# Kernel tuning notes

Measured on AMD Instinct MI355X. Metric: run time of the kernel, lower is better.

## Reference

```python
import jax, jax.numpy as jnp
import numpy as np

S_DIM, T_DIM, FEAT_DIM = 2048, 2048, 128
NCE_N, NCE_T, NCE_MOM = 16384, 0.07, 0.5
N_DATA, BATCH = 100000, 64
EPS = 1e-7


def _l2norm(x):
    return x / jnp.linalg.norm(x, axis=1, keepdims=True)


def setup_inputs() -> dict:
    key = jax.random.key(0)
    ks = jax.random.split(key, 10)
    feat_s = jax.random.normal(ks[0], (BATCH, S_DIM), dtype=jnp.float32)
    feat_t = jax.random.normal(ks[1], (BATCH, T_DIM), dtype=jnp.float32)
    idx = jax.random.randint(ks[2], (BATCH,), 0, N_DATA)
    sample_idx = jax.random.randint(ks[3], (BATCH, NCE_N + 1), 0, N_DATA)
    sample_idx = sample_idx.at[:, 0].set(idx)  # positive sample in column 0
    # Embed linear weights (Linear(dim_in, feat_dim))
    w_s = jax.random.normal(ks[4], (FEAT_DIM, S_DIM), dtype=jnp.float32) / np.sqrt(S_DIM)
    b_s = jnp.zeros((FEAT_DIM,), dtype=jnp.float32)
    w_t = jax.random.normal(ks[5], (FEAT_DIM, T_DIM), dtype=jnp.float32) / np.sqrt(T_DIM)
    b_t = jnp.zeros((FEAT_DIM,), dtype=jnp.float32)
    # memory banks, uniform(-stdv, stdv), stdv = 1/sqrt(feat_dim/3)
    stdv = 1.0 / np.sqrt(FEAT_DIM / 3.0)
    mem_v1 = jax.random.uniform(ks[6], (N_DATA, FEAT_DIM), dtype=jnp.float32, minval=-stdv, maxval=stdv)
    mem_v2 = jax.random.uniform(ks[7], (N_DATA, FEAT_DIM), dtype=jnp.float32, minval=-stdv, maxval=stdv)
    return {"feat_s": feat_s, "feat_t": feat_t, "idx": idx, "sample_idx": sample_idx,
            "w_s": w_s, "b_s": b_s, "w_t": w_t, "b_t": b_t,
            "mem_v1": mem_v1, "mem_v2": mem_v2}


def _contrast_out(mem, samp_idx, v):
    # gather [B, K+1, D] from memory bank, bmm against [B, D]
    w = mem[samp_idx]                                # [B, K+1, D]
    logits = jnp.einsum('bkd,bd->bk', w, v) / NCE_T  # [B, K+1]
    out = jnp.exp(logits)
    z = jnp.mean(out) * N_DATA                       # first-pass Z estimate
    return out / z


def _contrast_loss(x):
    b = x.shape[0]
    m = float(NCE_N) / N_DATA
    log_d1 = jnp.log(x[:, 0] / (x[:, 0] + m + EPS))          # positives
    log_d0 = jnp.log(m / (x[:, 1:] + m + EPS))               # negatives
    return -(jnp.sum(log_d1) + jnp.sum(log_d0)) / b


def reference(feat_s, feat_t, idx, sample_idx, w_s, b_s, w_t, b_t, mem_v1, mem_v2):
    hs = _l2norm(feat_s @ w_s.T + b_s)  # [B, D]
    ht = _l2norm(feat_t @ w_t.T + b_t)  # [B, D]
    out_s = _contrast_out(mem_v2, sample_idx, hs)  # anchor=student vs teacher memory
    out_t = _contrast_out(mem_v1, sample_idx, ht)  # anchor=teacher vs student memory
    return _contrast_loss(out_s) + _contrast_loss(out_t)
```

## Files before the change

### kernel.cpp

```cpp
#include <hip/hip_runtime.h>

#define DIM_IN   2048
#define FEAT     128
#define KP1      16385
#define NDATA    100000
#define BATCH    64
#define NBG      64
#define NTG      ((NDATA + NBG - 1) / NBG)
#define GCH      32
#define LCH      8

constexpr float NCE_T_INV = 1.0f / 0.07f;
constexpr float M_CONST   = 16384.0f / 100000.0f;
constexpr float EPS_C     = 1e-7f;

typedef short bf16x8 __attribute__((ext_vector_type(8)));
typedef float f32x4  __attribute__((ext_vector_type(4)));

#define VP_PLANE 34816
#define VP_SIDE  17408
#define VP_ROW   272

__global__ void __launch_bounds__(1024) embed_kernel(
    const float* __restrict__ feat_s, const float* __restrict__ feat_t,
    const float* __restrict__ w_s, const float* __restrict__ b_s,
    const float* __restrict__ w_t, const float* __restrict__ b_t,
    char* __restrict__ vplanes, float* __restrict__ z_zero,
    float* __restrict__ out_zero)
{
    const int blk  = blockIdx.x;
    const int side = blk >> 6;
    const int b    = blk & 63;
    const float* feat = (side == 0 ? feat_s : feat_t) + (size_t)b * DIM_IN;
    const float* w    = (side == 0 ? w_s : w_t);
    const float* bias = (side == 0 ? b_s : b_t);

    __shared__ float sfeat[DIM_IN];
    __shared__ float pre[FEAT];
    __shared__ float wsum[2];

    const int t = threadIdx.x;
    if (blk == 0) {
        if (t < 128) z_zero[t] = 0.f;
        else if (t == 128) out_zero[0] = 0.f;
    }
    {
        const float4* f4 = (const float4*)feat;
        float4* s4 = (float4*)sfeat;
        if (t < 512) s4[t] = f4[t];
    }
    __syncthreads();

    const int wv = t >> 6, ln = t & 63;
    const float4* w4  = (const float4*)w;
    const float4* sf4 = (const float4*)sfeat;
#pragma unroll 2
    for (int i = 0; i < 8; ++i) {
        const int d = wv + i * 16;
        float s = 0.f;
#pragma unroll
        for (int seg = 0; seg < 8; ++seg) {
            float4 a = w4[d * (DIM_IN / 4) + seg * 64 + ln];
            float4 f = sf4[seg * 64 + ln];
            s += a.x * f.x + a.y * f.y + a.z * f.z + a.w * f.w;
        }
#pragma unroll
        for (int o = 32; o > 0; o >>= 1) s += __shfl_xor(s, o, 64);
        if (ln == 0) pre[d] = s;
    }
    __syncthreads();

    if (t < 128) {
        float p = pre[t] + bias[t];
        pre[t] = p;
        float sq = p * p;
#pragma unroll
        for (int o = 32; o > 0; o >>= 1) sq += __shfl_xor(sq, o, 64);
        if ((t & 63) == 0) wsum[t >> 6] = sq;
    }
    __syncthreads();
    if (t < 128) {
        float inv_norm = 1.0f / sqrtf(wsum[0] + wsum[1]);
        float x = pre[t] * inv_norm;
        unsigned int u = __float_as_uint(x);
        unsigned short h = (unsigned short)(u >> 16);
        float hf = __uint_as_float(u & 0xffff0000u);
        float lr = x - hf;
        unsigned short l = (unsigned short)(__float_as_uint(lr) >> 16);
        const size_t off = (size_t)side * VP_SIDE + (size_t)b * VP_ROW + t * 2;
        *(unsigned short*)(vplanes + off)            = h;
        *(unsigned short*)(vplanes + VP_PLANE + off) = l;
    }
}

__global__ void __launch_bounds__(512) gemm_exp_kernel(
    const float* __restrict__ mem_v1, const float* __restrict__ mem_v2,
    const char* __restrict__ vplanes, float* __restrict__ E)
{
    __shared__ __align__(16) char lds[67584];

    const int bx   = blockIdx.x;
    const int side = bx & 1;
    const int tile = bx >> 1;
    const int n0   = tile * NBG;
    const float* bank = (side == 0 ? mem_v2 : mem_v1);
    const int t  = threadIdx.x;
    const int wv = t >> 6, ln = t & 63;
    const int lm = ln & 15;
    const int kb = ln >> 4;
    const int ntile = wv & 3;
    const int mhalf = wv >> 2;
    const int nloc  = ntile * 16 + lm;

    {
        const size_t bmax = (size_t)NDATA * 512 - 16;
        const char* bbase = (const char*)bank;
        for (int s = wv; s < 32; s += 8) {
            const int o   = s * 1024 + ln * 16;
            const int row = o >> 9;
            const int so  = (o & ~511) | ((o & 511) ^ ((row & 7) << 4));
            size_t g = (size_t)n0 * 512 + so;
            if (g > bmax) g = bmax;
            __builtin_amdgcn_global_load_lds(
                (const __attribute__((address_space(1))) void*)(bbase + g),
                (__attribute__((address_space(3))) void*)(lds + 34816 + s * 1024),
                16, 0, 0);
        }
    }
    {
        const char* hbase = vplanes + (size_t)side * VP_SIDE;
        const char* lbase = vplanes + VP_PLANE + (size_t)side * VP_SIDE;
        for (int seg = wv; seg < 34; seg += 8) {
            const char* src = (seg < 17 ? hbase + seg * 1024
                                        : lbase + (seg - 17) * 1024) + ln * 16;
            __builtin_amdgcn_global_load_lds(
                (const __attribute__((address_space(1))) void*)src,
                (__attribute__((address_space(3))) void*)(lds + seg * 1024),
                16, 0, 0);
        }
    }

    f32x4 acc[2];
    acc[0] = (f32x4){0.f, 0.f, 0.f, 0.f};
    acc[1] = (f32x4){0.f, 0.f, 0.f, 0.f};

    __syncthreads();

    const int sw = (nloc & 7) << 4;
#pragma unroll
    for (int c = 0; c < 4; ++c) {
        const int bofs = nloc * 512 + c * 128 + kb * 32;
        const float4 f0 = *(const float4*)(lds + 34816 + ((bofs)      ^ sw));
        const float4 f1 = *(const float4*)(lds + 34816 + ((bofs + 16) ^ sw));
        const float xs[8] = {f0.x, f0.y, f0.z, f0.w, f1.x, f1.y, f1.z, f1.w};
        bf16x8 bh, bl;
#pragma unroll
        for (int j = 0; j < 8; ++j) {
            unsigned int u = __float_as_uint(xs[j]);
            bh[j] = (short)(u >> 16);
            float hf = __uint_as_float(u & 0xffff0000u);
            bl[j] = (short)(__float_as_uint(xs[j] - hf) >> 16);
        }
#pragma unroll
        for (int i = 0; i < 2; ++i) {
            const int mi = mhalf * 2 + i;
            bf16x8 ah = *(const bf16x8*)(lds + (mi * 16 + lm) * VP_ROW + c * 64 + kb * 16);
            bf16x8 al = *(const bf16x8*)(lds + 17408 + (mi * 16 + lm) * VP_ROW + c * 64 + kb * 16);
            acc[i] = __builtin_amdgcn_mfma_f32_16x16x32_bf16(ah, bh, acc[i], 0, 0, 0);
            acc[i] = __builtin_amdgcn_mfma_f32_16x16x32_bf16(al, bh, acc[i], 0, 0, 0);
            acc[i] = __builtin_amdgcn_mfma_f32_16x16x32_bf16(ah, bl, acc[i], 0, 0, 0);
        }
    }

    const int nn = n0 + nloc;
    if (nn < NDATA) {
#pragma unroll
        for (int i = 0; i < 2; ++i) {
            const int mi = mhalf * 2 + i;
#pragma unroll
            for (int jj = 0; jj < 4; ++jj) {
                const int anchor = mi * 16 + kb * 4 + jj;
                E[(size_t)(side * 64 + anchor) * NDATA + nn] =
                    __expf(acc[i][jj] * NCE_T_INV);
            }
        }
    }
}

__global__ void __launch_bounds__(256) gather_z_kernel(
    const int* __restrict__ sample_idx, const float* __restrict__ E,
    float* __restrict__ ex_out, float* __restrict__ z_out)
{
    const int blk   = blockIdx.x;
    const int chunk = blk >> 7;
    const int sb    = blk & 127;
    const int b     = sb & 63;
    const float* Eb = E + (size_t)sb * NDATA;

    float zp = 0.f;
    for (int k = chunk * 256 + threadIdx.x; k < KP1; k += GCH * 256) {
        const int idx = sample_idx[(size_t)b * KP1 + k];
        const float e = Eb[idx];
        ex_out[(size_t)sb * KP1 + k] = e;
        zp += e;
    }
#pragma unroll
    for (int o = 32; o > 0; o >>= 1) zp += __shfl_xor(zp, o, 64);
    __shared__ float zw[4];
    if ((threadIdx.x & 63) == 0) zw[threadIdx.x >> 6] = zp;
    __syncthreads();
    if (threadIdx.x == 0) atomicAdd(&z_out[sb], zw[0] + zw[1] + zw[2] + zw[3]);
}

__global__ void __launch_bounds__(256) loss_kernel(
    const float* __restrict__ ex_in, const float* __restrict__ z_in,
    float* __restrict__ out)
{
    const int blk   = blockIdx.x;
    const int chunk = blk >> 7;
    const int sb    = blk & 127;
    const int side  = sb >> 6;

    __shared__ float zsh;
    if (threadIdx.x < 64) {
        float zv = z_in[side * 64 + threadIdx.x];
#pragma unroll
        for (int o = 32; o > 0; o >>= 1) zv += __shfl_xor(zv, o, 64);
        if (threadIdx.x == 0) zsh = zv;
    }
    __syncthreads();

    const float z  = zsh * ((float)NDATA / (64.0f * (float)KP1));
    const float rz = 1.0f / z;
    const float* ex = ex_in + (size_t)sb * KP1;

    float part = 0.f;
    for (int k = chunk * 256 + threadIdx.x; k < KP1; k += LCH * 256) {
        const float x = ex[k] * rz;
        if (k == 0) part += __logf(x / (x + M_CONST + EPS_C));
        else        part += __logf(M_CONST / (x + M_CONST + EPS_C));
    }
#pragma unroll
    for (int o = 32; o > 0; o >>= 1) part += __shfl_xor(part, o, 64);
    __shared__ float pw[4];
    if ((threadIdx.x & 63) == 0) pw[threadIdx.x >> 6] = part;
    __syncthreads();
    if (threadIdx.x == 0)
        atomicAdd(out, -(pw[0] + pw[1] + pw[2] + pw[3]) * (1.0f / 64.0f));
}

extern "C" void kernel_launch(void* const* d_in, const int* in_sizes, int n_in,
                              void* d_out, int out_size, void* d_ws, size_t ws_size,
                              hipStream_t stream)
{
    const float* feat_s     = (const float*)d_in[0];
    const float* feat_t     = (const float*)d_in[1];
    const int*   sample_idx = (const int*)  d_in[3];
    const float* w_s        = (const float*)d_in[4];
    const float* b_s        = (const float*)d_in[5];
    const float* w_t        = (const float*)d_in[6];
    const float* b_t        = (const float*)d_in[7];
    const float* mem_v1     = (const float*)d_in[8];
    const float* mem_v2     = (const float*)d_in[9];
    float* out = (float*)d_out;

    char*  ws     = (char*)d_ws;
    float* ws_z   = (float*)ws;
    float* ws_ex  = (float*)(ws + 512);
    char*  ws_vp  = (char*)(ws + 512);
    float* ws_E   = (float*)(ws + 512 + (size_t)2 * BATCH * KP1 * sizeof(float));

    embed_kernel<<<2 * BATCH, 1024, 0, stream>>>(feat_s, feat_t, w_s, b_s, w_t, b_t,
                                                 ws_vp, ws_z, out);
    gemm_exp_kernel<<<2 * NTG, 512, 0, stream>>>(mem_v1, mem_v2, ws_vp, ws_E);
    gather_z_kernel<<<2 * BATCH * GCH, 256, 0, stream>>>(sample_idx, ws_E, ws_ex, ws_z);
    loss_kernel<<<2 * BATCH * LCH, 256, 0, stream>>>(ws_ex, ws_z, out);
}
```

Measured before the change: 205.7 us.

## Shrink GEMM tile to 32 rows and share sample indices across both sides

The GEMM-exp kernel now processes 32 memory-bank rows per block with 256 threads instead of 64 rows with 512 threads, and drops the bounds clamp because 32 divides NDATA evenly. This gives more, smaller blocks with less LDS each, but every block still reloads the full 34 KB vplane tile, so the vplane traffic per row doubles. The gather and loss kernels now handle both sides (student and teacher) in one block per batch row, so each sample index is loaded once and used for two E lookups. This halves index reads and block count, at the cost of more work per thread.

```diff
diff --git a/kernel.cpp b/kernel.cpp
--- a/kernel.cpp
+++ b/kernel.cpp
@@ -5,8 +5,8 @@
 #define KP1      16385
 #define NDATA    100000
 #define BATCH    64
-#define NBG      64
-#define NTG      ((NDATA + NBG - 1) / NBG)
+#define NBG      32
+#define NTG      (NDATA / NBG)
 #define GCH      32
 #define LCH      8
 
@@ -93,11 +93,11 @@
     }
 }
 
-__global__ void __launch_bounds__(512) gemm_exp_kernel(
+__global__ void __launch_bounds__(256) gemm_exp_kernel(
     const float* __restrict__ mem_v1, const float* __restrict__ mem_v2,
     const char* __restrict__ vplanes, float* __restrict__ E)
 {
-    __shared__ __align__(16) char lds[67584];
+    __shared__ __align__(16) char lds[51200];
 
     const int bx   = blockIdx.x;
     const int side = bx & 1;
@@ -108,19 +108,17 @@
     const int wv = t >> 6, ln = t & 63;
     const int lm = ln & 15;
     const int kb = ln >> 4;
-    const int ntile = wv & 3;
-    const int mhalf = wv >> 2;
+    const int ntile = wv & 1;
+    const int mpair = wv >> 1;
     const int nloc  = ntile * 16 + lm;
 
     {
-        const size_t bmax = (size_t)NDATA * 512 - 16;
         const char* bbase = (const char*)bank;
-        for (int s = wv; s < 32; s += 8) {
+        for (int s = wv; s < 16; s += 4) {
             const int o   = s * 1024 + ln * 16;
             const int row = o >> 9;
             const int so  = (o & ~511) | ((o & 511) ^ ((row & 7) << 4));
-            size_t g = (size_t)n0 * 512 + so;
-            if (g > bmax) g = bmax;
+            const size_t g = (size_t)n0 * 512 + so;
             __builtin_amdgcn_global_load_lds(
                 (const __attribute__((address_space(1))) void*)(bbase + g),
                 (__attribute__((address_space(3))) void*)(lds + 34816 + s * 1024),
@@ -130,7 +128,7 @@
     {
         const char* hbase = vplanes + (size_t)side * VP_SIDE;
         const char* lbase = vplanes + VP_PLANE + (size_t)side * VP_SIDE;
-        for (int seg = wv; seg < 34; seg += 8) {
+        for (int seg = wv; seg < 34; seg += 4) {
             const char* src = (seg < 17 ? hbase + seg * 1024
                                         : lbase + (seg - 17) * 1024) + ln * 16;
             __builtin_amdgcn_global_load_lds(
@@ -163,7 +161,7 @@
         }
 #pragma unroll
         for (int i = 0; i < 2; ++i) {
-            const int mi = mhalf * 2 + i;
+            const int mi = mpair * 2 + i;
             bf16x8 ah = *(const bf16x8*)(lds + (mi * 16 + lm) * VP_ROW + c * 64 + kb * 16);
             bf16x8 al = *(const bf16x8*)(lds + 17408 + (mi * 16 + lm) * VP_ROW + c * 64 + kb * 16);
             acc[i] = __builtin_amdgcn_mfma_f32_16x16x32_bf16(ah, bh, acc[i], 0, 0, 0);
@@ -176,7 +174,7 @@
     if (nn < NDATA) {
 #pragma unroll
         for (int i = 0; i < 2; ++i) {
-            const int mi = mhalf * 2 + i;
+            const int mi = mpair * 2 + i;
 #pragma unroll
             for (int jj = 0; jj < 4; ++jj) {
                 const int anchor = mi * 16 + kb * 4 + jj;
@@ -192,24 +190,36 @@
     float* __restrict__ ex_out, float* __restrict__ z_out)
 {
     const int blk   = blockIdx.x;
-    const int chunk = blk >> 7;
-    const int sb    = blk & 127;
-    const int b     = sb & 63;
-    const float* Eb = E + (size_t)sb * NDATA;
-
-    float zp = 0.f;
+    const int chunk = blk >> 6;
+    const int b     = blk & 63;
+    const float* E0 = E + (size_t)b * NDATA;
+    const float* E1 = E + (size_t)(64 + b) * NDATA;
+
+    float zp0 = 0.f, zp1 = 0.f;
     for (int k = chunk * 256 + threadIdx.x; k < KP1; k += GCH * 256) {
         const int idx = sample_idx[(size_t)b * KP1 + k];
-        const float e = Eb[idx];
-        ex_out[(size_t)sb * KP1 + k] = e;
-        zp += e;
-    }
-#pragma unroll
-    for (int o = 32; o > 0; o >>= 1) zp += __shfl_xor(zp, o, 64);
-    __shared__ float zw[4];
-    if ((threadIdx.x & 63) == 0) zw[threadIdx.x >> 6] = zp;
-    __syncthreads();
-    if (threadIdx.x == 0) atomicAdd(&z_out[sb], zw[0] + zw[1] + zw[2] + zw[3]);
+        const float e0 = E0[idx];
+        const float e1 = E1[idx];
+        ex_out[(size_t)b * KP1 + k]        = e0;
+        ex_out[(size_t)(64 + b) * KP1 + k] = e1;
+        zp0 += e0;
+        zp1 += e1;
+    }
+#pragma unroll
+    for (int o = 32; o > 0; o >>= 1) {
+        zp0 += __shfl_xor(zp0, o, 64);
+        zp1 += __shfl_xor(zp1, o, 64);
+    }
+    __shared__ float zw0[4], zw1[4];
+    if ((threadIdx.x & 63) == 0) {
+        zw0[threadIdx.x >> 6] = zp0;
+        zw1[threadIdx.x >> 6] = zp1;
+    }
+    __syncthreads();
+    if (threadIdx.x == 0) {
+        atomicAdd(&z_out[b],      zw0[0] + zw0[1] + zw0[2] + zw0[3]);
+        atomicAdd(&z_out[64 + b], zw1[0] + zw1[1] + zw1[2] + zw1[3]);
+    }
 }
 
 __global__ void __launch_bounds__(256) loss_kernel(
@@ -217,28 +227,35 @@
     float* __restrict__ out)
 {
     const int blk   = blockIdx.x;
-    const int chunk = blk >> 7;
-    const int sb    = blk & 127;
-    const int side  = sb >> 6;
-
-    __shared__ float zsh;
-    if (threadIdx.x < 64) {
-        float zv = z_in[side * 64 + threadIdx.x];
+    const int chunk = blk >> 6;
+    const int b     = blk & 63;
+
+    __shared__ float zsh[2];
+    if (threadIdx.x < 128) {
+        float zv = z_in[threadIdx.x];
 #pragma unroll
         for (int o = 32; o > 0; o >>= 1) zv += __shfl_xor(zv, o, 64);
-        if (threadIdx.x == 0) zsh = zv;
-    }
-    __syncthreads();
-
-    const float z  = zsh * ((float)NDATA / (64.0f * (float)KP1));
-    const float rz = 1.0f / z;
-    const float* ex = ex_in + (size_t)sb * KP1;
+        if ((threadIdx.x & 63) == 0) zsh[threadIdx.x >> 6] = zv;
+    }
+    __syncthreads();
+
+    const float scale = (float)NDATA / (64.0f * (float)KP1);
+    const float rz0 = 1.0f / (zsh[0] * scale);
+    const float rz1 = 1.0f / (zsh[1] * scale);
+    const float* ex0 = ex_in + (size_t)b * KP1;
+    const float* ex1 = ex_in + (size_t)(64 + b) * KP1;
 
     float part = 0.f;
     for (int k = chunk * 256 + threadIdx.x; k < KP1; k += LCH * 256) {
-        const float x = ex[k] * rz;
-        if (k == 0) part += __logf(x / (x + M_CONST + EPS_C));
-        else        part += __logf(M_CONST / (x + M_CONST + EPS_C));
+        const float x0 = ex0[k] * rz0;
+        const float x1 = ex1[k] * rz1;
+        if (k == 0) {
+            part += __logf(x0 / (x0 + M_CONST + EPS_C));
+            part += __logf(x1 / (x1 + M_CONST + EPS_C));
+        } else {
+            part += __logf(M_CONST / (x0 + M_CONST + EPS_C));
+            part += __logf(M_CONST / (x1 + M_CONST + EPS_C));
+        }
     }
 #pragma unroll
     for (int o = 32; o > 0; o >>= 1) part += __shfl_xor(part, o, 64);
@@ -272,7 +289,7 @@
 
     embed_kernel<<<2 * BATCH, 1024, 0, stream>>>(feat_s, feat_t, w_s, b_s, w_t, b_t,
                                                  ws_vp, ws_z, out);
-    gemm_exp_kernel<<<2 * NTG, 512, 0, stream>>>(mem_v1, mem_v2, ws_vp, ws_E);
-    gather_z_kernel<<<2 * BATCH * GCH, 256, 0, stream>>>(sample_idx, ws_E, ws_ex, ws_z);
-    loss_kernel<<<2 * BATCH * LCH, 256, 0, stream>>>(ws_ex, ws_z, out);
-}
+    gemm_exp_kernel<<<2 * NTG, 256, 0, stream>>>(mem_v1, mem_v2, ws_vp, ws_E);
+    gather_z_kernel<<<BATCH * GCH, 256, 0, stream>>>(sample_idx, ws_E, ws_ex, ws_z);
+    loss_kernel<<<BATCH * LCH, 256, 0, stream>>>(ws_ex, ws_z, out);
+}
```

After: 204.0 us. About the same (-0.8%).
